# Optimization experiments

Measured on AMD Instinct MI355X. Metric: run time of the kernel, lower is better.

## Reference

```python
import jax, jax.numpy as jnp
import numpy as np

N = 8192
D_IN = 512
D_OUT = 512


def setup_inputs() -> dict:
    key = jax.random.key(0)
    k1, k2, k3, k4 = jax.random.split(key, 4)
    x = jax.random.normal(k1, (N, D_IN), dtype=jnp.float32)
    adj = jax.random.uniform(k2, (N, N), dtype=jnp.float32)
    # nn.Linear params: weight (out, in), bias (out,)
    bound = 1.0 / np.sqrt(D_IN)
    W = jax.random.uniform(k3, (D_OUT, D_IN), minval=-bound, maxval=bound, dtype=jnp.float32)
    b = jax.random.uniform(k4, (D_OUT,), minval=-bound, maxval=bound, dtype=jnp.float32)
    return {"x": x, "adj": adj, "W": W, "b": b}


def reference(x, adj, W, b):
    # Symmetric normalization: D^-1/2 (A + I) D^-1/2.
    # Original uses diag-matmuls; broadcast scaling is the identical math
    # without the O(n^3) diagonal GEMMs.
    a = adj + jnp.eye(adj.shape[0], dtype=adj.dtype)
    d = jnp.sum(a, axis=1) ** -0.5  # (N,)
    a_norm = d[:, None] * a * d[None, :]
    support = a_norm @ x                      # (N, D_IN)
    out = support @ W.T + b                   # (N, D_OUT)
    out = jax.nn.relu(out)
    # dropout: identity in eval/reference mode
    return out
```

## Files before the change

kernel.cpp:

```cpp
#include <hip/hip_runtime.h>
#include <stdint.h>

typedef __bf16 bf16_t;
typedef __bf16 bf16x8 __attribute__((ext_vector_type(8)));
typedef __bf16 bf16x4v __attribute__((ext_vector_type(4)));
typedef float f32x16 __attribute__((ext_vector_type(16)));

#define AS_GLOBAL __attribute__((address_space(1)))
#define AS_LDS    __attribute__((address_space(3)))

static constexpr int NN   = 8192;
static constexpr int DIN  = 512;
static constexpr int DOUT = 512;
static constexpr int SPLITK = 4;

__device__ __forceinline__ void async_cp16(const bf16_t* g, bf16_t* l) {
  __builtin_amdgcn_global_load_lds((AS_GLOBAL unsigned int*)g,
                                   (AS_LDS unsigned int*)l, 16, 0, 0);
}

__global__ __launch_bounds__(256) void k_rowsum_convert(
    const float* __restrict__ adj, const float* __restrict__ x,
    const float* __restrict__ W, bf16_t* __restrict__ adjb,
    bf16_t* __restrict__ dxb, bf16_t* __restrict__ Wb,
    float* __restrict__ d) {
  const int row = blockIdx.x;
  const int t = threadIdx.x;
  const float4* rf4 = (const float4*)(adj + (size_t)row * NN);
  bf16_t* outp = adjb + (size_t)row * NN;
  const int diagF4 = row >> 2;
  float sum = 0.f;
#pragma unroll
  for (int c = 0; c < 8; ++c) {
    int f4i = c * 256 + t;
    float4 a = rf4[f4i];
    sum += a.x + a.y + a.z + a.w;
    bf16x4v o;
    o[0] = (bf16_t)a.x; o[1] = (bf16_t)a.y; o[2] = (bf16_t)a.z; o[3] = (bf16_t)a.w;
    if (f4i == diagF4) {
      int s = row & 3;
      float vv = s == 0 ? a.x : s == 1 ? a.y : s == 2 ? a.z : a.w;
      o[s] = (bf16_t)(vv + 1.0f);
    }
    *(bf16x4v*)(outp + f4i * 4) = o;
  }
#pragma unroll
  for (int off = 32; off > 0; off >>= 1) sum += __shfl_down(sum, off);
  __shared__ float red[4];
  if ((t & 63) == 0) red[t >> 6] = sum;
  __syncthreads();
  const float s = rsqrtf(red[0] + red[1] + red[2] + red[3] + 1.0f);
  if (t == 0) d[row] = s;
  if (t < 128) {
    float4 v = *(const float4*)(x + (size_t)row * DIN + t * 4);
    bf16x4v o;
    o[0] = (bf16_t)(v.x * s); o[1] = (bf16_t)(v.y * s);
    o[2] = (bf16_t)(v.z * s); o[3] = (bf16_t)(v.w * s);
    *(bf16x4v*)(dxb + (size_t)row * DIN + t * 4) = o;
  } else if (t < 256 && row < DOUT) {
    int tt = t - 128;
    float4 v = *(const float4*)(W + (size_t)row * DIN + tt * 4);
    bf16x4v o;
    o[0] = (bf16_t)v.x; o[1] = (bf16_t)v.y; o[2] = (bf16_t)v.z; o[3] = (bf16_t)v.w;
    *(bf16x4v*)(Wb + (size_t)row * DIN + tt * 4) = o;
  }
}

__device__ __forceinline__ void gemm_tile_128x128_db(
    const bf16_t* __restrict__ A, const bf16_t* __restrict__ B,
    int lda, int ldb, int m0, int n0, int kStart, int kEnd,
    bf16_t* As, bf16_t* Bs, f32x16 acc[2][2]) {
  const int t = threadIdx.x;
  const int lane = t & 63;
  const int wid = t >> 6;
  const int wm = wid >> 1, wn = wid & 1;
  const int l32 = lane & 31, half = lane >> 5;

  const int swz = (t & 7) ^ ((t >> 3) & 7);
  const bf16_t* gA = A + (size_t)(m0 + (t >> 3)) * lda + swz * 8 + kStart;
  const bf16_t* gB = B + (size_t)(n0 + (t >> 3)) * ldb + swz * 8 + kStart;
  const int xorc = lane & 7;
  const int nIter = (kEnd - kStart) >> 6;

#pragma unroll
  for (int i = 0; i < 4; ++i) {
    async_cp16(gA + (size_t)(i * 32) * lda, As + t * 8 + i * 2048);
    async_cp16(gB + (size_t)(i * 32) * ldb, Bs + t * 8 + i * 2048);
  }
  gA += 64; gB += 64;

  int cur = 0;
  for (int it = 0; it < nIter; ++it) {
    if (it + 1 < nIter) {
      const int nb = (cur ^ 1) * 8192;
#pragma unroll
      for (int i = 0; i < 4; ++i) {
        async_cp16(gA + (size_t)(i * 32) * lda, As + nb + t * 8 + i * 2048);
        async_cp16(gB + (size_t)(i * 32) * ldb, Bs + nb + t * 8 + i * 2048);
      }
      gA += 64; gB += 64;
      asm volatile("s_waitcnt vmcnt(8)" ::: "memory");
    } else {
      asm volatile("s_waitcnt vmcnt(0)" ::: "memory");
    }
    __builtin_amdgcn_s_barrier();

    const bf16_t* Ab = As + cur * 8192;
    const bf16_t* Bb = Bs + cur * 8192;
#pragma unroll
    for (int ks = 0; ks < 4; ++ks) {
      const int pchunk = ((ks * 2 + half) ^ xorc) * 8;
      bf16x8 av[2], bv[2];
#pragma unroll
      for (int f = 0; f < 2; ++f) {
        av[f] = *(const bf16x8*)(Ab + (wm * 64 + f * 32 + l32) * 64 + pchunk);
        bv[f] = *(const bf16x8*)(Bb + (wn * 64 + f * 32 + l32) * 64 + pchunk);
      }
#pragma unroll
      for (int fm = 0; fm < 2; ++fm)
#pragma unroll
        for (int fn = 0; fn < 2; ++fn)
          acc[fm][fn] = __builtin_amdgcn_mfma_f32_32x32x16_bf16(
              av[fm], bv[fn], acc[fm][fn], 0, 0, 0);
    }
    asm volatile("s_waitcnt lgkmcnt(0)" ::: "memory");
    __builtin_amdgcn_s_barrier();
    cur ^= 1;
  }
}

__global__ __launch_bounds__(256) void k_gemmY(
    const bf16_t* __restrict__ Wb, const bf16_t* __restrict__ dxb,
    bf16_t* __restrict__ YT) {
  __shared__ __align__(16) bf16_t As[2 * 128 * 64];
  __shared__ __align__(16) bf16_t Bs[2 * 128 * 64];
  f32x16 acc[2][2];
#pragma unroll
  for (int a = 0; a < 2; ++a)
#pragma unroll
    for (int b = 0; b < 2; ++b)
#pragma unroll
      for (int r = 0; r < 16; ++r) acc[a][b][r] = 0.f;

  const int m0 = blockIdx.x * 128, n0 = blockIdx.y * 128;
  gemm_tile_128x128_db(Wb, dxb, DIN, DIN, m0, n0, 0, DIN, As, Bs, acc);

  const int t = threadIdx.x;
  const int lane = t & 63, wid = t >> 6;
  const int wm = wid >> 1, wn = wid & 1;
  const int l32 = lane & 31, half = lane >> 5;
#pragma unroll
  for (int fm = 0; fm < 2; ++fm)
#pragma unroll
    for (int fn = 0; fn < 2; ++fn) {
      int gc = n0 + wn * 64 + fn * 32 + l32;
#pragma unroll
      for (int reg = 0; reg < 16; ++reg) {
        int gr = m0 + wm * 64 + fm * 32 + (reg & 3) + 8 * (reg >> 2) + 4 * half;
        YT[(size_t)gr * NN + gc] = (bf16_t)acc[fm][fn][reg];
      }
    }
}

__global__ __launch_bounds__(512, 2) void k_gemm1(
    const bf16_t* __restrict__ adjb, const bf16_t* __restrict__ YT,
    float* __restrict__ part) {
  __shared__ __align__(16) bf16_t As[2 * 256 * 64];
  __shared__ __align__(16) bf16_t Bs[2 * 256 * 64];
  f32x16 acc[4][2];
#pragma unroll
  for (int a = 0; a < 4; ++a)
#pragma unroll
    for (int b = 0; b < 2; ++b)
#pragma unroll
      for (int r = 0; r < 16; ++r) acc[a][b][r] = 0.f;

  const int lin = blockIdx.x;
  const int c = (lin & 7) * 32 + (lin >> 3);
  const int n0 = (c & 1) * 256;
  const int m0 = ((c >> 1) & 31) * 256;
  const int kc = c >> 6;
  const int kStart = kc * (NN / SPLITK);
  const int nIter = (NN / SPLITK) >> 6;

  const int t = threadIdx.x;
  const int lane = t & 63;
  const int wid = t >> 6;
  const int wm = wid >> 2, wn = wid & 3;
  const int l32 = lane & 31, half = lane >> 5;
  const int xorc = lane & 7;

  const int swz = (t & 7) ^ ((t >> 3) & 7);
  const bf16_t* gA = adjb + (size_t)(m0 + (t >> 3)) * NN + swz * 8 + kStart;
  const bf16_t* gB = YT   + (size_t)(n0 + (t >> 3)) * NN + swz * 8 + kStart;

#pragma unroll
  for (int i = 0; i < 4; ++i) {
    async_cp16(gA + (size_t)(i * 64) * NN, As + t * 8 + i * 4096);
    async_cp16(gB + (size_t)(i * 64) * NN, Bs + t * 8 + i * 4096);
  }
  gA += 64; gB += 64;

  int cur = 0;
  for (int it = 0; it < nIter; ++it) {
    if (it + 1 < nIter) {
      const int nb = (cur ^ 1) * 16384;
#pragma unroll
      for (int i = 0; i < 4; ++i) {
        async_cp16(gA + (size_t)(i * 64) * NN, As + nb + t * 8 + i * 4096);
        async_cp16(gB + (size_t)(i * 64) * NN, Bs + nb + t * 8 + i * 4096);
      }
      gA += 64; gB += 64;
      asm volatile("s_waitcnt vmcnt(8)" ::: "memory");
    } else {
      asm volatile("s_waitcnt vmcnt(0)" ::: "memory");
    }
    __builtin_amdgcn_s_barrier();

    const bf16_t* Ab = As + cur * 16384;
    const bf16_t* Bb = Bs + cur * 16384;
#pragma unroll
    for (int ks = 0; ks < 4; ++ks) {
      const int pchunk = ((ks * 2 + half) ^ xorc) * 8;
      bf16x8 av[4], bv[2];
#pragma unroll
      for (int f = 0; f < 4; ++f)
        av[f] = *(const bf16x8*)(Ab + (wm * 128 + f * 32 + l32) * 64 + pchunk);
#pragma unroll
      for (int f = 0; f < 2; ++f)
        bv[f] = *(const bf16x8*)(Bb + (wn * 64 + f * 32 + l32) * 64 + pchunk);
#pragma unroll
      for (int fm = 0; fm < 4; ++fm)
#pragma unroll
        for (int fn = 0; fn < 2; ++fn)
          acc[fm][fn] = __builtin_amdgcn_mfma_f32_32x32x16_bf16(
              av[fm], bv[fn], acc[fm][fn], 0, 0, 0);
    }
    asm volatile("s_waitcnt lgkmcnt(0)" ::: "memory");
    __builtin_amdgcn_s_barrier();
    cur ^= 1;
  }

  float* outp = part + (size_t)kc * NN * DOUT;
#pragma unroll
  for (int fm = 0; fm < 4; ++fm)
#pragma unroll
    for (int fn = 0; fn < 2; ++fn) {
      int gc = n0 + wn * 64 + fn * 32 + l32;
#pragma unroll
      for (int reg = 0; reg < 16; ++reg) {
        int gr = m0 + wm * 128 + fm * 32 + (reg & 3) + 8 * (reg >> 2) + 4 * half;
        outp[(size_t)gr * DOUT + gc] = acc[fm][fn][reg];
      }
    }
}

__global__ __launch_bounds__(256) void k_out(
    const float* __restrict__ part, const float* __restrict__ d,
    const float* __restrict__ bias, float* __restrict__ outp) {
  int idx = blockIdx.x * 256 + threadIdx.x;
  int i = idx >> 7;
  int j4 = idx & 127;
  float4 p = *(const float4*)(part + (size_t)idx * 4);
#pragma unroll
  for (int kc = 1; kc < SPLITK; ++kc) {
    float4 q = *(const float4*)(part + (size_t)kc * NN * DOUT + (size_t)idx * 4);
    p.x += q.x; p.y += q.y; p.z += q.z; p.w += q.w;
  }
  float4 bb = *(const float4*)(bias + j4 * 4);
  float di = d[i];
  float4 o;
  o.x = fmaxf(fmaf(di, p.x, bb.x), 0.f);
  o.y = fmaxf(fmaf(di, p.y, bb.y), 0.f);
  o.z = fmaxf(fmaf(di, p.z, bb.z), 0.f);
  o.w = fmaxf(fmaf(di, p.w, bb.w), 0.f);
  *(float4*)(outp + (size_t)idx * 4) = o;
}

extern "C" void kernel_launch(void* const* d_in, const int* in_sizes, int n_in,
                              void* d_out, int out_size, void* d_ws, size_t ws_size,
                              hipStream_t stream) {
  const float* x   = (const float*)d_in[0];
  const float* adj = (const float*)d_in[1];
  const float* W   = (const float*)d_in[2];
  const float* b   = (const float*)d_in[3];
  float* out = (float*)d_out;

  char* ws = (char*)d_ws;
  bf16_t* adjb = (bf16_t*)(ws);
  float*  part = (float*)(ws + 134217728);
  bf16_t* YT   = (bf16_t*)(ws + 201326592);
  bf16_t* dxb  = (bf16_t*)(ws + 209715200);
  bf16_t* Wb   = (bf16_t*)(ws + 218103808);
  float*  dvec = (float*)(ws + 218628096);

  k_rowsum_convert<<<NN, 256, 0, stream>>>(adj, x, W, adjb, dxb, Wb, dvec);
  k_gemmY<<<dim3(DOUT / 128, NN / 128), 256, 0, stream>>>(Wb, dxb, YT);
  k_gemm1<<<(NN / 256) * (DOUT / 256) * SPLITK, 512, 0, stream>>>(adjb, YT, part);
  k_out<<<(NN * DOUT) / 1024, 256, 0, stream>>>(part, dvec, b, out);
}
```

Baseline: 507.9 us.

## Deepen GEMM1 pipeline to four-stage K=32 ring buffer with setprio

Reworks the main adjacency GEMM loop from a double buffer with K=64 tiles into a 4-deep ring of K=32 tiles, keeping three stages of loads in flight. It adds a new XOR swizzle for the narrower tiles, raises wave priority around the MFMA block, and drops to one workgroup per CU per launch bounds. The aim is to hide global-load latency better and issue one barrier per stage. The cost is lower occupancy, more barriers per K, and a fragile hand-counted vmcnt schedule.

```diff
diff --git a/kernel.cpp b/kernel.cpp
--- a/kernel.cpp
+++ b/kernel.cpp
@@ -162,11 +162,11 @@
     }
 }
 
-__global__ __launch_bounds__(512, 2) void k_gemm1(
+__global__ __launch_bounds__(512, 1) void k_gemm1(
     const bf16_t* __restrict__ adjb, const bf16_t* __restrict__ YT,
     float* __restrict__ part) {
-  __shared__ __align__(16) bf16_t As[2 * 256 * 64];
-  __shared__ __align__(16) bf16_t Bs[2 * 256 * 64];
+  __shared__ __align__(16) bf16_t As[4 * 8192];
+  __shared__ __align__(16) bf16_t Bs[4 * 8192];
   f32x16 acc[4][2];
 #pragma unroll
   for (int a = 0; a < 4; ++a)
@@ -181,54 +181,47 @@
   const int m0 = ((c >> 1) & 31) * 256;
   const int kc = c >> 6;
   const int kStart = kc * (NN / SPLITK);
-  const int nIter = (NN / SPLITK) >> 6;
 
   const int t = threadIdx.x;
   const int lane = t & 63;
   const int wid = t >> 6;
   const int wm = wid >> 2, wn = wid & 3;
   const int l32 = lane & 31, half = lane >> 5;
-  const int xorc = lane & 7;
-
-  const int swz = (t & 7) ^ ((t >> 3) & 7);
-  const bf16_t* gA = adjb + (size_t)(m0 + (t >> 3)) * NN + swz * 8 + kStart;
-  const bf16_t* gB = YT   + (size_t)(n0 + (t >> 3)) * NN + swz * 8 + kStart;
-
-#pragma unroll
-  for (int i = 0; i < 4; ++i) {
-    async_cp16(gA + (size_t)(i * 64) * NN, As + t * 8 + i * 4096);
-    async_cp16(gB + (size_t)(i * 64) * NN, Bs + t * 8 + i * 4096);
-  }
-  gA += 64; gB += 64;
-
-  int cur = 0;
-  for (int it = 0; it < nIter; ++it) {
-    if (it + 1 < nIter) {
-      const int nb = (cur ^ 1) * 16384;
-#pragma unroll
-      for (int i = 0; i < 4; ++i) {
-        async_cp16(gA + (size_t)(i * 64) * NN, As + nb + t * 8 + i * 4096);
-        async_cp16(gB + (size_t)(i * 64) * NN, Bs + nb + t * 8 + i * 4096);
-      }
-      gA += 64; gB += 64;
-      asm volatile("s_waitcnt vmcnt(8)" ::: "memory");
-    } else {
-      asm volatile("s_waitcnt vmcnt(0)" ::: "memory");
-    }
-    __builtin_amdgcn_s_barrier();
-
-    const bf16_t* Ab = As + cur * 16384;
-    const bf16_t* Bb = Bs + cur * 16384;
-#pragma unroll
-    for (int ks = 0; ks < 4; ++ks) {
-      const int pchunk = ((ks * 2 + half) ^ xorc) * 8;
+  const int sread = (l32 >> 1) & 3;
+
+  const int g = (t & 3) ^ ((t >> 3) & 3);
+  const bf16_t* gA = adjb + (size_t)(m0 + (t >> 2)) * NN + g * 8 + kStart;
+  const bf16_t* gB = YT   + (size_t)(n0 + (t >> 2)) * NN + g * 8 + kStart;
+
+  auto stage = [&](int buf, int kk) {
+#pragma unroll
+    for (int i = 0; i < 2; ++i) {
+      async_cp16(gA + (size_t)(i * 128) * NN + kk, As + buf * 8192 + i * 4096 + t * 8);
+      async_cp16(gB + (size_t)(i * 128) * NN + kk, Bs + buf * 8192 + i * 4096 + t * 8);
+    }
+  };
+
+  stage(0, 0); stage(1, 32); stage(2, 64);
+  asm volatile("s_waitcnt vmcnt(8)" ::: "memory");
+  __builtin_amdgcn_s_barrier();
+
+  for (int u = 0; u < 64; ++u) {
+    if (u + 3 < 64) stage((u + 3) & 3, (u + 3) * 32);
+
+    const bf16_t* Ab = As + (u & 3) * 8192;
+    const bf16_t* Bb = Bs + (u & 3) * 8192;
+    __builtin_amdgcn_s_setprio(1);
+#pragma unroll
+    for (int ks = 0; ks < 2; ++ks) {
+      const int q = ks * 2 + half;
+      const int pc = (q ^ sread) * 8;
       bf16x8 av[4], bv[2];
 #pragma unroll
       for (int f = 0; f < 4; ++f)
-        av[f] = *(const bf16x8*)(Ab + (wm * 128 + f * 32 + l32) * 64 + pchunk);
+        av[f] = *(const bf16x8*)(Ab + (wm * 128 + f * 32 + l32) * 32 + pc);
 #pragma unroll
       for (int f = 0; f < 2; ++f)
-        bv[f] = *(const bf16x8*)(Bb + (wn * 64 + f * 32 + l32) * 64 + pchunk);
+        bv[f] = *(const bf16x8*)(Bb + (wn * 64 + f * 32 + l32) * 32 + pc);
 #pragma unroll
       for (int fm = 0; fm < 4; ++fm)
 #pragma unroll
@@ -236,9 +229,12 @@
           acc[fm][fn] = __builtin_amdgcn_mfma_f32_32x32x16_bf16(
               av[fm], bv[fn], acc[fm][fn], 0, 0, 0);
     }
+    __builtin_amdgcn_s_setprio(0);
     asm volatile("s_waitcnt lgkmcnt(0)" ::: "memory");
+    if (u < 61)       asm volatile("s_waitcnt vmcnt(8)" ::: "memory");
+    else if (u == 61) asm volatile("s_waitcnt vmcnt(4)" ::: "memory");
+    else              asm volatile("s_waitcnt vmcnt(0)" ::: "memory");
     __builtin_amdgcn_s_barrier();
-    cur ^= 1;
   }
 
   float* outp = part + (size_t)kc * NN * DOUT;
```

After: 520.9 us. 1.03x slower.
